# Performance work log

Hardware: AMD Instinct MI355X
Metric: run time of the kernel (lower is better)

The kernel has to match this reference:

```python
import jax, jax.numpy as jnp
import numpy as np

B, T, D, H = 4, 1024, 2048, 16
E = D // H  # head_dim = 128


def setup_inputs() -> dict:
    key = jax.random.key(0)
    ks = jax.random.split(key, 10)
    s = 1.0 / np.sqrt(D)
    x = jax.random.normal(ks[0], (B, T, D), dtype=jnp.float32)
    attention_mask = jnp.ones((B, T), dtype=jnp.int32)
    # Per-head q/k/v projections stacked along head axis: [H, E, D] weights, [H, E] biases.
    Wq = jax.random.uniform(ks[1], (H, E, D), jnp.float32, -s, s)
    bq = jax.random.uniform(ks[2], (H, E), jnp.float32, -s, s)
    Wk = jax.random.uniform(ks[3], (H, E, D), jnp.float32, -s, s)
    bk = jax.random.uniform(ks[4], (H, E), jnp.float32, -s, s)
    Wv = jax.random.uniform(ks[5], (H, E, D), jnp.float32, -s, s)
    bv = jax.random.uniform(ks[6], (H, E), jnp.float32, -s, s)
    Wo = jax.random.uniform(ks[7], (D, D), jnp.float32, -s, s)
    bo = jax.random.uniform(ks[8], (D,), jnp.float32, -s, s)
    return {"x": x, "attention_mask": attention_mask, "Wq": Wq, "bq": bq,
            "Wk": Wk, "bk": bk, "Wv": Wv, "bv": bv, "Wo": Wo, "bo": bo}


def _causal_mask(Tq, Tk, dtype):
    neg = jnp.finfo(dtype).min
    qi = jnp.arange(Tq)[:, None]
    ki = jnp.arange(Tk)[None, :]
    max_allowed = Tk - Tq + qi
    return jnp.where(ki > max_allowed, neg, jnp.zeros((), dtype)).astype(dtype)


def reference(x, attention_mask, Wq, bq, Wk, bk, Wv, bv, Wo, bo):
    dt = x.dtype
    neg = jnp.finfo(dt).min
    scale = 1.0 / np.sqrt(E)
    # per-head projections (vectorized over heads): [B,H,T,E]
    q = jnp.einsum('btd,hed->bhte', x, Wq) + bq[None, :, None, :]
    k = jnp.einsum('btd,hed->bhte', x, Wk) + bk[None, :, None, :]
    v = jnp.einsum('btd,hed->bhte', x, Wv) + bv[None, :, None, :]
    # scores [B,H,Tq,Tk]
    scores = jnp.einsum('bhqe,bhke->bhqk', q, k) * scale
    scores = scores + _causal_mask(T, T, dt)[None, None]
    keep = attention_mask.astype(bool)  # [B,Tk]
    scores = jnp.where(keep[:, None, None, :], scores, neg)
    probs = jax.nn.softmax(scores, axis=-1)
    y = jnp.einsum('bhqk,bhke->bhqe', probs, v)  # [B,H,T,E]
    # heads concatenated along feature dim in head order
    y = jnp.transpose(y, (0, 2, 1, 3)).reshape(B, T, D)
    out = y @ Wo.T + bo
    return out
```

## Files before the change

### kernel.cpp

```cpp
#include <hip/hip_runtime.h>
#include <hip/hip_bf16.h>


typedef __attribute__((ext_vector_type(4))) float f32x4;
typedef __attribute__((ext_vector_type(8))) short s16x8;
typedef __attribute__((ext_vector_type(4))) unsigned short us16x4;
typedef __attribute__((ext_vector_type(8))) unsigned short us16x8;

#define Bd 4
#define Td 1024
#define Dd 2048
#define Hd 16
#define Ed 128

__device__ __forceinline__ unsigned short f2bf(float f) {
  unsigned int u = __builtin_bit_cast(unsigned int, f);
  u = (u + 0x7fffu + ((u >> 16) & 1u)) >> 16;
  return (unsigned short)u;
}

__device__ __forceinline__ void gload_lds16(const void* g, void* l) {
  __builtin_amdgcn_global_load_lds(
      (const __attribute__((address_space(1))) unsigned int*)g,
      (__attribute__((address_space(3))) unsigned int*)l, 16, 0, 0);
}

__global__ void cvt_f32_bf16(const float* __restrict__ in,
                             unsigned short* __restrict__ out, int n4) {
  int i = blockIdx.x * 256 + threadIdx.x;
  if (i >= n4) return;
  float4 v = reinterpret_cast<const float4*>(in)[i];
  us16x4 o = {f2bf(v.x), f2bf(v.y), f2bf(v.z), f2bf(v.w)};
  reinterpret_cast<us16x4*>(out)[i] = o;
}

__global__ void bias_concat(const float* __restrict__ bq, const float* __restrict__ bk,
                            const float* __restrict__ bv, float* __restrict__ out) {
  int i = blockIdx.x * 256 + threadIdx.x;
  const float* s = (i < 2048) ? bq : ((i < 4096) ? bk : bv);
  out[i] = s[i & 2047];
}

template <int OUT_BF16>
__global__ __launch_bounds__(256, 2) void gemm_bt(
    const unsigned short* __restrict__ A, const unsigned short* __restrict__ Bm,
    const float* __restrict__ bias, void* __restrict__ C, int M, int N, int K) {
  __shared__ unsigned short As[8192];
  __shared__ unsigned short Bs[8192];
  const int tid = threadIdx.x;
  const int lane = tid & 63, w = tid >> 6;
  const int g = lane >> 4, m15 = lane & 15;
  const int wr = w >> 1, wc = w & 1;
  const int row0 = blockIdx.y * 128, col0 = blockIdx.x * 128;

  f32x4 acc[4][4] = {};
  const int nK = K >> 6;
  for (int kt = 0; kt < nK; ++kt) {
    const int k0 = kt << 6;
    __syncthreads();
#pragma unroll
    for (int i = 0; i < 4; ++i) {
      const int p = w * 256 + i * 64 + lane;
      const int prow = p >> 3;
      const int lslot = (p & 7) ^ (prow & 7);
      gload_lds16(A + (size_t)(row0 + prow) * K + k0 + lslot * 8,
                  &As[(size_t)(w * 256 + i * 64) * 8]);
      gload_lds16(Bm + (size_t)(col0 + prow) * K + k0 + lslot * 8,
                  &Bs[(size_t)(w * 256 + i * 64) * 8]);
    }
    __syncthreads();
#pragma unroll
    for (int ks = 0; ks < 2; ++ks) {
      s16x8 af[4], bf[4];
#pragma unroll
      for (int i = 0; i < 4; ++i) {
        const int r = wr * 64 + i * 16 + m15;
        af[i] = *reinterpret_cast<const s16x8*>(&As[(r * 8 + ((ks * 4 + g) ^ (r & 7))) * 8]);
      }
#pragma unroll
      for (int j = 0; j < 4; ++j) {
        const int r = wc * 64 + j * 16 + m15;
        bf[j] = *reinterpret_cast<const s16x8*>(&Bs[(r * 8 + ((ks * 4 + g) ^ (r & 7))) * 8]);
      }
#pragma unroll
      for (int i = 0; i < 4; ++i)
#pragma unroll
        for (int j = 0; j < 4; ++j)
          acc[i][j] = __builtin_amdgcn_mfma_f32_16x16x32_bf16(af[i], bf[j], acc[i][j], 0, 0, 0);
    }
  }
#pragma unroll
  for (int j = 0; j < 4; ++j) {
    const int col = col0 + wc * 64 + j * 16 + m15;
    const float bv = bias[col];
#pragma unroll
    for (int i = 0; i < 4; ++i)
#pragma unroll
      for (int r = 0; r < 4; ++r) {
        const int row = row0 + wr * 64 + i * 16 + g * 4 + r;
        const float v = acc[i][j][r] + bv;
        if (OUT_BF16)
          ((unsigned short*)C)[(size_t)row * N + col] = f2bf(v);
        else
          ((float*)C)[(size_t)row * N + col] = v;
      }
  }
}

__global__ void transpose_v(const unsigned short* __restrict__ QKV,
                            unsigned short* __restrict__ Vt) {
  const int bh = blockIdx.y;
  const int t0 = blockIdx.x * 64;
  const int b = bh >> 4, h = bh & 15;
  const int tid = threadIdx.x;
  const unsigned short* src = QKV + (size_t)(b * Td) * 6144 + 4096 + h * 128;
  unsigned short* dst = Vt + (size_t)bh * 128 * Td;
#pragma unroll
  for (int kk = 0; kk < 4; ++kk) {
    const int c = tid + kk * 256;
    const int e = c >> 3, tc = c & 7;
    us16x8 v;
#pragma unroll
    for (int j = 0; j < 8; ++j)
      v[j] = src[(size_t)(t0 + tc * 8 + j) * 6144 + e];
    *reinterpret_cast<us16x8*>(&dst[(size_t)e * Td + t0 + tc * 8]) = v;
  }
}

__global__ __launch_bounds__(256, 2) void attn(
    const unsigned short* __restrict__ QKV, const unsigned short* __restrict__ Vt,
    const int* __restrict__ amask, unsigned short* __restrict__ Y) {
  __shared__ unsigned short Ks[4096];
  __shared__ unsigned short Vs[4096];
  __shared__ unsigned short Ps[4096];
  const int qt = blockIdx.x, bh = blockIdx.y;
  const int b = bh >> 4, h = bh & 15;
  const int q0 = qt * 128;
  const int tid = threadIdx.x, lane = tid & 63, w = tid >> 6;
  const int g = lane >> 4, m15 = lane & 15;
  const float scale = 0.08838834764831845f;

  s16x8 qf[2][4];
#pragma unroll
  for (int qr = 0; qr < 2; ++qr)
#pragma unroll
    for (int c = 0; c < 4; ++c)
      qf[qr][c] = *reinterpret_cast<const s16x8*>(
          &QKV[(size_t)(b * Td + q0 + w * 32 + qr * 16 + m15) * 6144 + h * 128 + c * 32 + g * 8]);

  f32x4 yacc[2][8] = {};
  float mrow[2][4], lrow[2][4];
#pragma unroll
  for (int qr = 0; qr < 2; ++qr)
#pragma unroll
    for (int r = 0; r < 4; ++r) { mrow[qr][r] = -1e30f; lrow[qr][r] = 0.f; }

  const int nkt = (q0 + 128) >> 5;
  for (int kt = 0; kt < nkt; ++kt) {
    const int k0 = kt << 5;
    __syncthreads();
#pragma unroll
    for (int i = 0; i < 2; ++i) {
      const int p = w * 128 + i * 64 + lane;
      {
        const int prow = p >> 4;
        const int lslot = (p & 15) ^ (prow & 7);
        gload_lds16(QKV + (size_t)(b * Td + k0 + prow) * 6144 + 2048 + h * 128 + lslot * 8,
                    &Ks[(size_t)(w * 128 + i * 64) * 8]);
      }
      {
        const int e = p >> 2;
        const int lslot = (p & 3) ^ (e & 3);
        gload_lds16(Vt + (size_t)(bh * 128 + e) * Td + k0 + lslot * 8,
                    &Vs[(size_t)(w * 128 + i * 64) * 8]);
      }
    }
    __syncthreads();

    f32x4 sf[2][2] = {};
#pragma unroll
    for (int kc = 0; kc < 2; ++kc)
#pragma unroll
      for (int c = 0; c < 4; ++c) {
        const int krow = kc * 16 + m15;
        const s16x8 kf = *reinterpret_cast<const s16x8*>(
            &Ks[(krow * 16 + ((c * 4 + g) ^ (krow & 7))) * 8]);
#pragma unroll
        for (int qr = 0; qr < 2; ++qr)
          sf[qr][kc] = __builtin_amdgcn_mfma_f32_16x16x32_bf16(qf[qr][c], kf, sf[qr][kc], 0, 0, 0);
      }

#pragma unroll
    for (int kc = 0; kc < 2; ++kc) {
      const int kgl = k0 + kc * 16 + m15;
      const int amv = amask[b * Td + kgl];
#pragma unroll
      for (int qr = 0; qr < 2; ++qr)
#pragma unroll
        for (int r = 0; r < 4; ++r) {
          const int qg = q0 + w * 32 + qr * 16 + g * 4 + r;
          const float s = sf[qr][kc][r] * scale;
          sf[qr][kc][r] = (kgl <= qg && amv != 0) ? s : -1e30f;
        }
    }

#pragma unroll
    for (int qr = 0; qr < 2; ++qr) {
      float al[4];
#pragma unroll
      for (int r = 0; r < 4; ++r) {
        float t = fmaxf(sf[qr][0][r], sf[qr][1][r]);
        t = fmaxf(t, __shfl_xor(t, 1));
        t = fmaxf(t, __shfl_xor(t, 2));
        t = fmaxf(t, __shfl_xor(t, 4));
        t = fmaxf(t, __shfl_xor(t, 8));
        const float mn = fmaxf(mrow[qr][r], t);
        al[r] = __expf(mrow[qr][r] - mn);
        mrow[qr][r] = mn;
        const float p0 = __expf(sf[qr][0][r] - mn);
        const float p1 = __expf(sf[qr][1][r] - mn);
        sf[qr][0][r] = p0;
        sf[qr][1][r] = p1;
        float rs = p0 + p1;
        rs += __shfl_xor(rs, 1);
        rs += __shfl_xor(rs, 2);
        rs += __shfl_xor(rs, 4);
        rs += __shfl_xor(rs, 8);
        lrow[qr][r] = lrow[qr][r] * al[r] + rs;
      }
#pragma unroll
      for (int n = 0; n < 8; ++n)
#pragma unroll
        for (int r = 0; r < 4; ++r) yacc[qr][n][r] *= al[r];
    }

    unsigned short* pw = &Ps[w * 1024];
#pragma unroll
    for (int qr = 0; qr < 2; ++qr)
#pragma unroll
      for (int kc = 0; kc < 2; ++kc) {
        const int kc3 = kc * 2 + (m15 >> 3), j = m15 & 7;
#pragma unroll
        for (int r = 0; r < 4; ++r)
          pw[(kc3 * 32 + qr * 16 + g * 4 + r) * 8 + j] = f2bf(sf[qr][kc][r]);
      }
    asm volatile("s_waitcnt lgkmcnt(0)" ::: "memory");
    __builtin_amdgcn_sched_barrier(0);
    s16x8 pf[2];
#pragma unroll
    for (int qr = 0; qr < 2; ++qr)
      pf[qr] = *reinterpret_cast<const s16x8*>(&pw[(g * 32 + qr * 16 + m15) * 8]);

#pragma unroll
    for (int n = 0; n < 8; ++n) {
      const int e = n * 16 + m15;
      const s16x8 vf = *reinterpret_cast<const s16x8*>(&Vs[(e * 4 + (g ^ (e & 3))) * 8]);
      yacc[0][n] = __builtin_amdgcn_mfma_f32_16x16x32_bf16(pf[0], vf, yacc[0][n], 0, 0, 0);
      yacc[1][n] = __builtin_amdgcn_mfma_f32_16x16x32_bf16(pf[1], vf, yacc[1][n], 0, 0, 0);
    }
  }

#pragma unroll
  for (int qr = 0; qr < 2; ++qr)
#pragma unroll
    for (int r = 0; r < 4; ++r) {
      const float inv = 1.0f / lrow[qr][r];
      const size_t rowoff = (size_t)(b * Td + q0 + w * 32 + qr * 16 + g * 4 + r) * Dd + h * Ed;
#pragma unroll
      for (int n = 0; n < 8; ++n)
        Y[rowoff + n * 16 + m15] = f2bf(yacc[qr][n][r] * inv);
    }
}

extern "C" void kernel_launch(void* const* d_in, const int* in_sizes, int n_in,
                              void* d_out, int out_size, void* d_ws, size_t ws_size,
                              hipStream_t stream) {
  const float* x = (const float*)d_in[0];
  const int* amask = (const int*)d_in[1];
  const float* Wq = (const float*)d_in[2];
  const float* bq = (const float*)d_in[3];
  const float* Wk = (const float*)d_in[4];
  const float* bk = (const float*)d_in[5];
  const float* Wv = (const float*)d_in[6];
  const float* bv = (const float*)d_in[7];
  const float* Wo = (const float*)d_in[8];
  const float* bo = (const float*)d_in[9];
  float* out = (float*)d_out;

  char* ws = (char*)d_ws;
  unsigned short* wqkv = (unsigned short*)(ws);
  unsigned short* xbf  = (unsigned short*)(ws + 25165824);
  unsigned short* qkv  = (unsigned short*)(ws + 41943040);
  unsigned short* wobf = (unsigned short*)(ws + 92274688);
  float* bqkv          = (float*)(ws + 100663296);
  unsigned short* vt   = wqkv;
  unsigned short* ybuf = xbf;

  cvt_f32_bf16<<<8192, 256, 0, stream>>>(x, xbf, 2097152);
  cvt_f32_bf16<<<4096, 256, 0, stream>>>(Wq, wqkv, 1048576);
  cvt_f32_bf16<<<4096, 256, 0, stream>>>(Wk, wqkv + 4194304, 1048576);
  cvt_f32_bf16<<<4096, 256, 0, stream>>>(Wv, wqkv + 8388608, 1048576);
  cvt_f32_bf16<<<4096, 256, 0, stream>>>(Wo, wobf, 1048576);
  bias_concat<<<24, 256, 0, stream>>>(bq, bk, bv, bqkv);

  gemm_bt<1><<<dim3(48, 32), 256, 0, stream>>>(xbf, wqkv, bqkv, (void*)qkv, 4096, 6144, 2048);
  transpose_v<<<dim3(16, 64), 256, 0, stream>>>(qkv, vt);
  attn<<<dim3(8, 64), 256, 0, stream>>>(qkv, vt, amask, ybuf);
  gemm_bt<0><<<dim3(16, 32), 256, 0, stream>>>(ybuf, wobf, bo, (void*)out, 4096, 2048, 2048);
}
```

Measured before the change: 415.7 us.

## Fuse V transpose into QKV GEMM epilogue and rebalance causal attention

Result: no change. 409.8 us (-1.4%).

```diff
diff --git a/kernel.cpp b/kernel.cpp
--- a/kernel.cpp
+++ b/kernel.cpp
@@ -5,13 +5,9 @@
 typedef __attribute__((ext_vector_type(4))) float f32x4;
 typedef __attribute__((ext_vector_type(8))) short s16x8;
 typedef __attribute__((ext_vector_type(4))) unsigned short us16x4;
-typedef __attribute__((ext_vector_type(8))) unsigned short us16x8;
-
-#define Bd 4
+
 #define Td 1024
 #define Dd 2048
-#define Hd 16
-#define Ed 128
 
 __device__ __forceinline__ unsigned short f2bf(float f) {
   unsigned int u = __builtin_bit_cast(unsigned int, f);
@@ -41,10 +37,11 @@
   out[i] = s[i & 2047];
 }
 
-template <int OUT_BF16>
+template <int MODE>
 __global__ __launch_bounds__(256, 2) void gemm_bt(
     const unsigned short* __restrict__ A, const unsigned short* __restrict__ Bm,
-    const float* __restrict__ bias, void* __restrict__ C, int M, int N, int K) {
+    const float* __restrict__ bias, void* __restrict__ C,
+    unsigned short* __restrict__ Cv, int M, int N, int K, int ldc) {
   __shared__ unsigned short As[8192];
   __shared__ unsigned short Bs[8192];
   const int tid = threadIdx.x;
@@ -89,187 +86,210 @@
           acc[i][j] = __builtin_amdgcn_mfma_f32_16x16x32_bf16(af[i], bf[j], acc[i][j], 0, 0, 0);
     }
   }
-#pragma unroll
-  for (int j = 0; j < 4; ++j) {
-    const int col = col0 + wc * 64 + j * 16 + m15;
-    const float bv = bias[col];
-#pragma unroll
-    for (int i = 0; i < 4; ++i)
-#pragma unroll
-      for (int r = 0; r < 4; ++r) {
-        const int row = row0 + wr * 64 + i * 16 + g * 4 + r;
-        const float v = acc[i][j][r] + bv;
-        if (OUT_BF16)
-          ((unsigned short*)C)[(size_t)row * N + col] = f2bf(v);
-        else
-          ((float*)C)[(size_t)row * N + col] = v;
-      }
-  }
-}
-
-__global__ void transpose_v(const unsigned short* __restrict__ QKV,
-                            unsigned short* __restrict__ Vt) {
-  const int bh = blockIdx.y;
-  const int t0 = blockIdx.x * 64;
+  if (MODE == 1 && col0 >= 4096) {
+    const int vc0 = col0 - 4096;
+#pragma unroll
+    for (int j = 0; j < 4; ++j) {
+      const int vcol = vc0 + wc * 64 + j * 16 + m15;
+      const float bv = bias[4096 + vcol];
+      const int hh = vcol >> 7, e = vcol & 127;
+#pragma unroll
+      for (int i = 0; i < 4; ++i) {
+        const int row = row0 + wr * 64 + i * 16 + g * 4;
+        const int bb = row >> 10, tt = row & 1023;
+        us16x4 pk;
+#pragma unroll
+        for (int r = 0; r < 4; ++r) pk[r] = f2bf(acc[i][j][r] + bv);
+        *reinterpret_cast<us16x4*>(&Cv[((size_t)((bb * 16 + hh) * 128 + e)) * Td + tt]) = pk;
+      }
+    }
+  } else {
+#pragma unroll
+    for (int j = 0; j < 4; ++j) {
+      const int col = col0 + wc * 64 + j * 16 + m15;
+      const float bv = bias[col];
+#pragma unroll
+      for (int i = 0; i < 4; ++i)
+#pragma unroll
+        for (int r = 0; r < 4; ++r) {
+          const int row = row0 + wr * 64 + i * 16 + g * 4 + r;
+          const float v = acc[i][j][r] + bv;
+          if (MODE)
+            ((unsigned short*)C)[(size_t)row * ldc + col] = f2bf(v);
+          else
+            ((float*)C)[(size_t)row * ldc + col] = v;
+        }
+    }
+  }
+}
+
+#define SCALE 0.08838834764831845f
+
+#define GRP_SOFTMAX(SF, G, QB)                                                 \
+  {                                                                            \
+    _Pragma("unroll") for (int kc = 0; kc < 4; ++kc) {                         \
+      const int kgl = k0 + kc * 16 + m15;                                      \
+      const int okm = am[kc];                                                  \
+      _Pragma("unroll") for (int r = 0; r < 4; ++r) {                          \
+        const int qg = (QB) + g * 4 + r;                                       \
+        SF[kc][r] = (okm && kgl <= qg) ? SF[kc][r] * SCALE : -3.0e38f;         \
+      }                                                                        \
+    }                                                                          \
+    _Pragma("unroll") for (int r = 0; r < 4; ++r) {                            \
+      float t = fmaxf(fmaxf(SF[0][r], SF[1][r]), fmaxf(SF[2][r], SF[3][r]));   \
+      t = fmaxf(t, __shfl_xor(t, 1));                                          \
+      t = fmaxf(t, __shfl_xor(t, 2));                                          \
+      t = fmaxf(t, __shfl_xor(t, 4));                                          \
+      t = fmaxf(t, __shfl_xor(t, 8));                                          \
+      const float mn = fmaxf(mrow[G][r], t);                                   \
+      const float al = __expf(mrow[G][r] - mn);                                \
+      mrow[G][r] = mn;                                                         \
+      float rs = 0.f;                                                          \
+      _Pragma("unroll") for (int kc = 0; kc < 4; ++kc) {                       \
+        SF[kc][r] = __expf(SF[kc][r] - mn);                                    \
+        rs += SF[kc][r];                                                       \
+      }                                                                        \
+      rs += __shfl_xor(rs, 1);                                                 \
+      rs += __shfl_xor(rs, 2);                                                 \
+      rs += __shfl_xor(rs, 4);                                                 \
+      rs += __shfl_xor(rs, 8);                                                 \
+      lrow[G][r] = lrow[G][r] * al + rs;                                       \
+      _Pragma("unroll") for (int n = 0; n < 8; ++n) yacc[G][n][r] *= al;       \
+    }                                                                          \
+    _Pragma("unroll") for (int kc = 0; kc < 4; ++kc)                           \
+        _Pragma("unroll") for (int r = 0; r < 4; ++r) {                        \
+      const int prow = (G) * 16 + g * 4 + r;                                   \
+      pw[prow * 64 + ((kc * 16 + m15) ^ ((prow & 7) << 3))] = f2bf(SF[kc][r]); \
+    }                                                                          \
+  }
+
+__global__ __launch_bounds__(256, 2) void attn(
+    const unsigned short* __restrict__ qk, const unsigned short* __restrict__ vt,
+    const int* __restrict__ amask, unsigned short* __restrict__ Y) {
+  __shared__ unsigned short Ks[2][8192];
+  __shared__ unsigned short Vs[2][8192];
+  __shared__ unsigned short Ps[4][2048];
+  const int d = blockIdx.y * 8 + blockIdx.x;
+  const int wk = (d & 7) * 64 + (d >> 3);
+  const int p = wk & 7, bh = wk >> 3;
   const int b = bh >> 4, h = bh & 15;
-  const int tid = threadIdx.x;
-  const unsigned short* src = QKV + (size_t)(b * Td) * 6144 + 4096 + h * 128;
-  unsigned short* dst = Vt + (size_t)bh * 128 * Td;
-#pragma unroll
-  for (int kk = 0; kk < 4; ++kk) {
-    const int c = tid + kk * 256;
-    const int e = c >> 3, tc = c & 7;
-    us16x8 v;
-#pragma unroll
-    for (int j = 0; j < 8; ++j)
-      v[j] = src[(size_t)(t0 + tc * 8 + j) * 6144 + e];
-    *reinterpret_cast<us16x8*>(&dst[(size_t)e * Td + t0 + tc * 8]) = v;
-  }
-}
-
-__global__ __launch_bounds__(256, 2) void attn(
-    const unsigned short* __restrict__ QKV, const unsigned short* __restrict__ Vt,
-    const int* __restrict__ amask, unsigned short* __restrict__ Y) {
-  __shared__ unsigned short Ks[4096];
-  __shared__ unsigned short Vs[4096];
-  __shared__ unsigned short Ps[4096];
-  const int qt = blockIdx.x, bh = blockIdx.y;
-  const int b = bh >> 4, h = bh & 15;
-  const int q0 = qt * 128;
+  const int ta = p, tb = 15 - p;
   const int tid = threadIdx.x, lane = tid & 63, w = tid >> 6;
   const int g = lane >> 4, m15 = lane & 15;
-  const float scale = 0.08838834764831845f;
+  const int qab = ta * 64 + w * 16, qbb = tb * 64 + w * 16;
+  unsigned short* pw = Ps[w];
 
   s16x8 qf[2][4];
 #pragma unroll
-  for (int qr = 0; qr < 2; ++qr)
+  for (int G = 0; G < 2; ++G) {
+    const int qb_ = G ? qbb : qab;
 #pragma unroll
     for (int c = 0; c < 4; ++c)
-      qf[qr][c] = *reinterpret_cast<const s16x8*>(
-          &QKV[(size_t)(b * Td + q0 + w * 32 + qr * 16 + m15) * 6144 + h * 128 + c * 32 + g * 8]);
+      qf[G][c] = *reinterpret_cast<const s16x8*>(
+          &qk[(size_t)(b * Td + qb_ + m15) * 4096 + h * 128 + c * 32 + g * 8]);
+  }
 
   f32x4 yacc[2][8] = {};
   float mrow[2][4], lrow[2][4];
 #pragma unroll
-  for (int qr = 0; qr < 2; ++qr)
-#pragma unroll
-    for (int r = 0; r < 4; ++r) { mrow[qr][r] = -1e30f; lrow[qr][r] = 0.f; }
-
-  const int nkt = (q0 + 128) >> 5;
+  for (int G = 0; G < 2; ++G)
+#pragma unroll
+    for (int r = 0; r < 4; ++r) { mrow[G][r] = -3.0e38f; lrow[G][r] = 0.f; }
+
+  auto stage = [&](int buf, int kt) {
+    const int k0s = kt << 6;
+#pragma unroll
+    for (int i = 0; i < 4; ++i) {
+      const int pc = i * 256 + tid;
+      const int krow = pc >> 4;
+      const int ls = (pc & 15) ^ (krow & 7);
+      gload_lds16(qk + (size_t)(b * Td + k0s + krow) * 4096 + 2048 + h * 128 + ls * 8,
+                  &Ks[buf][(size_t)(i * 256 + w * 64) * 8]);
+      const int e = pc >> 3;
+      const int lv = (pc & 7) ^ (e & 7);
+      gload_lds16(vt + (size_t)(bh * 128 + e) * Td + k0s + lv * 8,
+                  &Vs[buf][(size_t)(i * 256 + w * 64) * 8]);
+    }
+  };
+
+  const int nkt = tb + 1;
+  stage(0, 0);
+  asm volatile("s_waitcnt vmcnt(0)" ::: "memory");
+  __syncthreads();
+  int cur = 0;
   for (int kt = 0; kt < nkt; ++kt) {
-    const int k0 = kt << 5;
-    __syncthreads();
-#pragma unroll
-    for (int i = 0; i < 2; ++i) {
-      const int p = w * 128 + i * 64 + lane;
-      {
-        const int prow = p >> 4;
-        const int lslot = (p & 15) ^ (prow & 7);
-        gload_lds16(QKV + (size_t)(b * Td + k0 + prow) * 6144 + 2048 + h * 128 + lslot * 8,
-                    &Ks[(size_t)(w * 128 + i * 64) * 8]);
-      }
-      {
-        const int e = p >> 2;
-        const int lslot = (p & 3) ^ (e & 3);
-        gload_lds16(Vt + (size_t)(bh * 128 + e) * Td + k0 + lslot * 8,
-                    &Vs[(size_t)(w * 128 + i * 64) * 8]);
-      }
-    }
-    __syncthreads();
-
-    f32x4 sf[2][2] = {};
-#pragma unroll
-    for (int kc = 0; kc < 2; ++kc)
+    const int k0 = kt << 6;
+    const bool actA = (kt <= ta);
+    if (kt + 1 < nkt) stage(cur ^ 1, kt + 1);
+    int am[4];
+#pragma unroll
+    for (int kc = 0; kc < 4; ++kc) am[kc] = amask[b * Td + k0 + kc * 16 + m15];
+
+    f32x4 sf0[4] = {}, sf1[4] = {};
+    __builtin_amdgcn_s_setprio(1);
+#pragma unroll
+    for (int kc = 0; kc < 4; ++kc) {
+      const int krow = kc * 16 + m15;
 #pragma unroll
       for (int c = 0; c < 4; ++c) {
-        const int krow = kc * 16 + m15;
         const s16x8 kf = *reinterpret_cast<const s16x8*>(
-            &Ks[(krow * 16 + ((c * 4 + g) ^ (krow & 7))) * 8]);
-#pragma unroll
-        for (int qr = 0; qr < 2; ++qr)
-          sf[qr][kc] = __builtin_amdgcn_mfma_f32_16x16x32_bf16(qf[qr][c], kf, sf[qr][kc], 0, 0, 0);
-      }
-
-#pragma unroll
-    for (int kc = 0; kc < 2; ++kc) {
-      const int kgl = k0 + kc * 16 + m15;
-      const int amv = amask[b * Td + kgl];
-#pragma unroll
-      for (int qr = 0; qr < 2; ++qr)
-#pragma unroll
-        for (int r = 0; r < 4; ++r) {
-          const int qg = q0 + w * 32 + qr * 16 + g * 4 + r;
-          const float s = sf[qr][kc][r] * scale;
-          sf[qr][kc][r] = (kgl <= qg && amv != 0) ? s : -1e30f;
-        }
-    }
-
-#pragma unroll
-    for (int qr = 0; qr < 2; ++qr) {
-      float al[4];
-#pragma unroll
-      for (int r = 0; r < 4; ++r) {
-        float t = fmaxf(sf[qr][0][r], sf[qr][1][r]);
-        t = fmaxf(t, __shfl_xor(t, 1));
-        t = fmaxf(t, __shfl_xor(t, 2));
-        t = fmaxf(t, __shfl_xor(t, 4));
-        t = fmaxf(t, __shfl_xor(t, 8));
-        const float mn = fmaxf(mrow[qr][r], t);
-        al[r] = __expf(mrow[qr][r] - mn);
-        mrow[qr][r] = mn;
-        const float p0 = __expf(sf[qr][0][r] - mn);
-        const float p1 = __expf(sf[qr][1][r] - mn);
-        sf[qr][0][r] = p0;
-        sf[qr][1][r] = p1;
-        float rs = p0 + p1;
-        rs += __shfl_xor(rs, 1);
-        rs += __shfl_xor(rs, 2);
-        rs += __shfl_xor(rs, 4);
-        rs += __shfl_xor(rs, 8);
-        lrow[qr][r] = lrow[qr][r] * al[r] + rs;
-      }
-#pragma unroll
-      for (int n = 0; n < 8; ++n)
-#pragma unroll
-        for (int r = 0; r < 4; ++r) yacc[qr][n][r] *= al[r];
-    }
-
-    unsigned short* pw = &Ps[w * 1024];
-#pragma unroll
-    for (int qr = 0; qr < 2; ++qr)
-#pragma unroll
-      for (int kc = 0; kc < 2; ++kc) {
-        const int kc3 = kc * 2 + (m15 >> 3), j = m15 & 7;
-#pragma unroll
-        for (int r = 0; r < 4; ++r)
-          pw[(kc3 * 32 + qr * 16 + g * 4 + r) * 8 + j] = f2bf(sf[qr][kc][r]);
-      }
+            &Ks[cur][(krow * 16 + ((c * 4 + g) ^ (krow & 7))) * 8]);
+        if (actA) sf0[kc] = __builtin_amdgcn_mfma_f32_16x16x32_bf16(qf[0][c], kf, sf0[kc], 0, 0, 0);
+        sf1[kc] = __builtin_amdgcn_mfma_f32_16x16x32_bf16(qf[1][c], kf, sf1[kc], 0, 0, 0);
+      }
+    }
+    __builtin_amdgcn_s_setprio(0);
+
+    if (actA) GRP_SOFTMAX(sf0, 0, qab)
+    GRP_SOFTMAX(sf1, 1, qbb)
+
     asm volatile("s_waitcnt lgkmcnt(0)" ::: "memory");
     __builtin_amdgcn_sched_barrier(0);
-    s16x8 pf[2];
-#pragma unroll
-    for (int qr = 0; qr < 2; ++qr)
-      pf[qr] = *reinterpret_cast<const s16x8*>(&pw[(g * 32 + qr * 16 + m15) * 8]);
-
+    s16x8 pa0[2], pa1[2];
+    if (actA) {
+#pragma unroll
+      for (int kcc = 0; kcc < 2; ++kcc)
+        pa0[kcc] = *reinterpret_cast<const s16x8*>(
+            &pw[m15 * 64 + ((kcc * 32 + g * 8) ^ ((m15 & 7) << 3))]);
+    }
+#pragma unroll
+    for (int kcc = 0; kcc < 2; ++kcc) {
+      const int prow = 16 + m15;
+      pa1[kcc] = *reinterpret_cast<const s16x8*>(
+          &pw[prow * 64 + ((kcc * 32 + g * 8) ^ ((prow & 7) << 3))]);
+    }
+
+    __builtin_amdgcn_s_setprio(1);
 #pragma unroll
     for (int n = 0; n < 8; ++n) {
       const int e = n * 16 + m15;
-      const s16x8 vf = *reinterpret_cast<const s16x8*>(&Vs[(e * 4 + (g ^ (e & 3))) * 8]);
-      yacc[0][n] = __builtin_amdgcn_mfma_f32_16x16x32_bf16(pf[0], vf, yacc[0][n], 0, 0, 0);
-      yacc[1][n] = __builtin_amdgcn_mfma_f32_16x16x32_bf16(pf[1], vf, yacc[1][n], 0, 0, 0);
-    }
-  }
-
-#pragma unroll
-  for (int qr = 0; qr < 2; ++qr)
+#pragma unroll
+      for (int kcc = 0; kcc < 2; ++kcc) {
+        const s16x8 vf = *reinterpret_cast<const s16x8*>(
+            &Vs[cur][(e * 8 + ((kcc * 4 + g) ^ (e & 7))) * 8]);
+        if (actA) yacc[0][n] = __builtin_amdgcn_mfma_f32_16x16x32_bf16(pa0[kcc], vf, yacc[0][n], 0, 0, 0);
+        yacc[1][n] = __builtin_amdgcn_mfma_f32_16x16x32_bf16(pa1[kcc], vf, yacc[1][n], 0, 0, 0);
+      }
+    }
+    __builtin_amdgcn_s_setprio(0);
+
+    asm volatile("s_waitcnt vmcnt(0)" ::: "memory");
+    __syncthreads();
+    cur ^= 1;
+  }
+
+#pragma unroll
+  for (int G = 0; G < 2; ++G) {
+    const int qb_ = G ? qbb : qab;
 #pragma unroll
     for (int r = 0; r < 4; ++r) {
-      const float inv = 1.0f / lrow[qr][r];
-      const size_t rowoff = (size_t)(b * Td + q0 + w * 32 + qr * 16 + g * 4 + r) * Dd + h * Ed;
+      const float inv = 1.0f / lrow[G][r];
+      const size_t rowoff = (size_t)(b * Td + qb_ + g * 4 + r) * Dd + h * 128;
 #pragma unroll
       for (int n = 0; n < 8; ++n)
-        Y[rowoff + n * 16 + m15] = f2bf(yacc[qr][n][r] * inv);
-    }
+        Y[rowoff + n * 16 + m15] = f2bf(yacc[G][n][r] * inv);
+    }
+  }
 }
 
 extern "C" void kernel_launch(void* const* d_in, const int* in_sizes, int n_in,
@@ -290,10 +310,10 @@
   char* ws = (char*)d_ws;
   unsigned short* wqkv = (unsigned short*)(ws);
   unsigned short* xbf  = (unsigned short*)(ws + 25165824);
-  unsigned short* qkv  = (unsigned short*)(ws + 41943040);
+  unsigned short* qk   = (unsigned short*)(ws + 41943040);
+  unsigned short* vt   = (unsigned short*)(ws + 75497472);
   unsigned short* wobf = (unsigned short*)(ws + 92274688);
   float* bqkv          = (float*)(ws + 100663296);
-  unsigned short* vt   = wqkv;
   unsigned short* ybuf = xbf;
 
   cvt_f32_bf16<<<8192, 256, 0, stream>>>(x, xbf, 2097152);
@@ -303,8 +323,7 @@
   cvt_f32_bf16<<<4096, 256, 0, stream>>>(Wo, wobf, 1048576);
   bias_concat<<<24, 256, 0, stream>>>(bq, bk, bv, bqkv);
 
-  gemm_bt<1><<<dim3(48, 32), 256, 0, stream>>>(xbf, wqkv, bqkv, (void*)qkv, 4096, 6144, 2048);
-  transpose_v<<<dim3(16, 64), 256, 0, stream>>>(qkv, vt);
-  attn<<<dim3(8, 64), 256, 0, stream>>>(qkv, vt, amask, ybuf);
-  gemm_bt<0><<<dim3(16, 32), 256, 0, stream>>>(ybuf, wobf, bo, (void*)out, 4096, 2048, 2048);
-}
+  gemm_bt<1><<<dim3(48, 32), 256, 0, stream>>>(xbf, wqkv, bqkv, (void*)qk, vt, 4096, 6144, 2048, 4096);
+  attn<<<dim3(8, 64), 256, 0, stream>>>(qk, vt, amask, ybuf);
+  gemm_bt<0><<<dim3(16, 32), 256, 0, stream>>>(ybuf, wobf, bo, (void*)out, nullptr, 4096, 2048, 2048, 2048);
+}
```
